# Optimization experiments

Hardware: AMD Instinct MI355X
Metric: run time of the kernel (lower is better)

Reference implementation:

```python
import jax, jax.numpy as jnp
import numpy as np

B, E, F, Q = 8, 2000, 6000, 20
D = 256   # entity_dim == word_dim (required: word_embedding output feeds LSTM with input_size=word_dim)
WD = 256
L = 3
NUM_ENTITY, NUM_REL, NUM_WORD = 400000, 6000, 60000
NNZ = 2 * B * F
PAGERANK_LAMBDA, FACT_SCALE = 0.8, 3.0
VERY_NEG = -100000000000.0
VERY_SMALL = 1e-10


def _lin(x, W, b):
    return x @ W.T + b


def _sparse_bmm(indices, values, x, num_rows):
    # indices: [3, nnz] = (batch, row, col); x: [B, C, Dx] -> out [B, num_rows, Dx]
    b, r, c = indices[0], indices[1], indices[2]
    contrib = values[:, None] * x[b, c]
    seg = b * num_rows + r
    out = jax.ops.segment_sum(contrib, seg, num_segments=x.shape[0] * num_rows)
    return out.reshape(x.shape[0], num_rows, x.shape[2])


def _lstm(x, Wih, Whh, bih, bhh):
    # PyTorch LSTM, batch_first, 1 layer, unidirectional; gate order i,f,g,o
    Bb, T, _ = x.shape
    H = Whh.shape[1]
    def step(carry, xt):
        h, c = carry
        g = xt @ Wih.T + bih + h @ Whh.T + bhh
        i, f, gg, o = jnp.split(g, 4, axis=-1)
        c = jax.nn.sigmoid(f) * c + jax.nn.sigmoid(i) * jnp.tanh(gg)
        h = jax.nn.sigmoid(o) * jnp.tanh(c)
        return (h, c), h
    init = (jnp.zeros((Bb, H), x.dtype), jnp.zeros((Bb, H), x.dtype))
    (h, c), hs = jax.lax.scan(step, init, jnp.swapaxes(x, 0, 1))
    return jnp.swapaxes(hs, 0, 1), h


def setup_inputs():
    key = jax.random.key(0)
    ks = iter(jax.random.split(key, 48))
    p = lambda shape: jax.random.normal(next(ks), shape, jnp.float32) * 0.02
    inp = {}
    inp['local_entity'] = jax.random.randint(next(ks), (B, E), 0, NUM_ENTITY + 1)
    inp['q2e_adj_mat'] = (jax.random.uniform(next(ks), (B, E, 1)) < 0.01).astype(jnp.float32)
    inp['kb_fact_rel'] = jax.random.randint(next(ks), (B, F), 0, NUM_REL)
    inp['query_text'] = jax.random.randint(next(ks), (B, Q), 0, NUM_WORD)
    inp['answer_dist'] = (jax.random.uniform(next(ks), (B, E)) < 0.005).astype(jnp.float32)
    eb = jax.random.randint(next(ks), (NNZ,), 0, B)
    ef = jax.random.randint(next(ks), (NNZ,), 0, F)
    ee = jax.random.randint(next(ks), (NNZ,), 0, E)
    inp['e2f_indices'] = jnp.stack([eb, ef, ee])
    inp['e2f_val'] = jnp.ones((NNZ,), jnp.float32)
    fb = jax.random.randint(next(ks), (NNZ,), 0, B)
    fe = jax.random.randint(next(ks), (NNZ,), 0, E)
    ff = jax.random.randint(next(ks), (NNZ,), 0, F)
    inp['f2e_indices'] = jnp.stack([fb, fe, ff])
    inp['f2e_val'] = jnp.ones((NNZ,), jnp.float32)
    inp['entity_table'] = p((NUM_ENTITY + 1, WD)).at[-1].set(0.0)
    inp['ent_lin_W'] = p((D, WD)); inp['ent_lin_b'] = jnp.zeros((D,), jnp.float32)
    inp['relation_table'] = p((NUM_REL + 1, WD)).at[-1].set(0.0)
    inp['rel_lin_W'] = p((D, WD)); inp['rel_lin_b'] = jnp.zeros((D,), jnp.float32)
    inp['word_table'] = p((NUM_WORD + 1, D)).at[-1].set(0.0)
    inp['lstm_Wih'] = p((4 * D, WD)); inp['lstm_Whh'] = p((4 * D, D))
    inp['lstm_bih'] = jnp.zeros((4 * D,), jnp.float32); inp['lstm_bhh'] = jnp.zeros((4 * D,), jnp.float32)
    inp['q2e_W'] = p((L, D, D)); inp['q2e_b'] = jnp.zeros((L, D), jnp.float32)
    inp['e2q_W'] = p((L, D, 3 * D)); inp['e2q_b'] = jnp.zeros((L, D), jnp.float32)
    inp['e2e_W'] = p((L, D, 3 * D)); inp['e2e_b'] = jnp.zeros((L, D), jnp.float32)
    inp['head_W'] = p((L, D, D)); inp['head_b'] = jnp.zeros((L, D), jnp.float32)
    inp['tail_W'] = p((L, D, D)); inp['tail_b'] = jnp.zeros((L, D), jnp.float32)
    inp['self_W'] = p((L, D, D)); inp['self_b'] = jnp.zeros((L, D), jnp.float32)
    inp['score_W'] = p((1, D)); inp['score_b'] = jnp.zeros((1,), jnp.float32)
    return inp


def reference(local_entity, q2e_adj_mat, kb_fact_rel, query_text, answer_dist, e2f_indices, e2f_val, f2e_indices, f2e_val, entity_table, ent_lin_W, ent_lin_b, relation_table, rel_lin_W, rel_lin_b, word_table, lstm_Wih, lstm_Whh, lstm_bih, lstm_bhh, q2e_W, q2e_b, e2q_W, e2q_b, e2e_W, e2e_b, head_W, head_b, tail_W, tail_b, self_W, self_b, score_W, score_b):
    query_mask = (query_text != NUM_WORD).astype(jnp.float32)          # [B,Q]
    local_entity_mask = (local_entity != NUM_ENTITY).astype(jnp.float32)
    # query encoder (dropout = identity in eval)
    query_hidden, h_last = _lstm(word_table[query_text], lstm_Wih, lstm_Whh, lstm_bih, lstm_bhh)
    query_node_emb = h_last[:, None, :]                                # [B,1,D]
    local_fact_emb = _lin(relation_table[kb_fact_rel], rel_lin_W, rel_lin_b)  # [B,F,D]
    div = jnp.sqrt(jnp.float32(D))
    sim = jnp.einsum('bqd,bfd->bqf', query_hidden, local_fact_emb) / div
    sim = jax.nn.softmax(sim + (1.0 - query_mask)[:, :, None] * VERY_NEG, axis=1)
    att = jnp.einsum('bqf,bqd->bfd', sim, query_hidden)
    Wt = jnp.sum(att * local_fact_emb, axis=2) / div                   # [B,F]
    W_tilde = jnp.exp(Wt - jnp.max(Wt, axis=1, keepdims=True))
    e2fT = jnp.stack([e2f_indices[0], e2f_indices[2], e2f_indices[1]])  # transpose(1,2)
    e2f_softmax = _sparse_bmm(e2fT, e2f_val, W_tilde[:, :, None], E)[..., 0]
    e2f_softmax = jnp.maximum(e2f_softmax, VERY_SMALL)
    pagerank_f = q2e_adj_mat[..., 0]                                    # [B,E]
    local_entity_emb = _lin(entity_table[local_entity], ent_lin_W, ent_lin_b)  # [B,E,D]
    for i in range(L):
        q2e_emb = jnp.broadcast_to(_lin(query_node_emb, q2e_W[i], q2e_b[i]), (B, E, D))
        nxt = jnp.concatenate([local_entity_emb, q2e_emb], axis=2)
        e2f_emb = jax.nn.relu(_lin(local_fact_emb, self_W[i], self_b[i]) + _sparse_bmm(e2f_indices, e2f_val, _lin(local_entity_emb, head_W[i], head_b[i]), F))
        e2f_norm = W_tilde[:, :, None] * _sparse_bmm(e2f_indices, e2f_val, (pagerank_f / e2f_softmax)[:, :, None], F)
        e2f_emb = e2f_emb * e2f_norm
        f2e_emb = jax.nn.relu(_lin(local_entity_emb, self_W[i], self_b[i]) + _sparse_bmm(f2e_indices, f2e_val, _lin(e2f_emb, tail_W[i], tail_b[i]), E))
        pagerank_f = PAGERANK_LAMBDA * _sparse_bmm(f2e_indices, f2e_val, e2f_norm, E)[..., 0] + (1.0 - PAGERANK_LAMBDA) * pagerank_f
        nxt = jnp.concatenate([nxt, FACT_SCALE * f2e_emb], axis=2)      # [B,E,3D]
        query_node_emb = jnp.einsum('be,bed->bd', pagerank_f, _lin(nxt, e2q_W[i], e2q_b[i]))[:, None, :]
        local_entity_emb = jax.nn.relu(_lin(nxt, e2e_W[i], e2e_b[i]))
    score = _lin(local_entity_emb, score_W, score_b)[..., 0]            # [B,E]
    loss = jnp.mean(jnp.maximum(score, 0.0) - score * answer_dist + jnp.log1p(jnp.exp(-jnp.abs(score))))
    score_m = score + (1.0 - local_entity_mask) * VERY_NEG
    pred = jnp.argmax(score_m, axis=1)
    pred_dist = jax.nn.sigmoid(score_m) * local_entity_mask
    return (loss, pred, pred_dist)
```

## Files before the change

kernel.cpp:

```cpp
#include <hip/hip_runtime.h>
#include <math.h>

#define BB 8
#define EE 2000
#define FF 6000
#define QQ 20
#define DD 256
#define NENT 400000
#define NWORD 60000
#define NNZ_ 96000
#define VNEG  (-1e11f)
#define VSMALL 1e-10f

typedef __attribute__((ext_vector_type(8))) short short8v;
typedef __attribute__((ext_vector_type(4))) short short4v;
typedef __attribute__((ext_vector_type(4))) float f32x4;

__device__ __forceinline__ unsigned short f2bf_rne(float x)
{
    unsigned u = __float_as_uint(x);
    u += 0x7FFFu + ((u >> 16) & 1u);
    return (unsigned short)(u >> 16);
}
__device__ __forceinline__ float bf2f(unsigned short h)
{
    return __uint_as_float((unsigned)h << 16);
}

template<int GATHER, int DUALW, int RELU, int RS, int BIASB>
__device__ __forceinline__ void mgemm_body(
    const float* __restrict__ A1, const int* __restrict__ idx,
    const float* __restrict__ A2, float sA2,
    const short* __restrict__ W1h, const short* __restrict__ W1l,
    const short* __restrict__ W2h, const short* __restrict__ W2l,
    const float* __restrict__ biasA,
    const float* __restrict__ rowscale, const float* __restrict__ bias2,
    float* __restrict__ out, int by, int bx,
    short* __restrict__ Ah, short* __restrict__ Al)
{
    const int tid = threadIdx.x;
    const int lane = tid & 63, wv = tid >> 6;
    const int wrow = wv >> 1, wcol = wv & 1;
    const int row0 = by * 128, col0 = bx * 64;

    const int sr = tid >> 1;
    const int sko = (tid & 1) << 5;
    const int grow = row0 + sr;
    const float* aRow1 = GATHER ? A1 + (size_t)idx[grow] * 256 : A1 + (size_t)grow * 256;
    const float* aRow2 = DUALW ? A2 + (size_t)grow * 256 : nullptr;

    f32x4 acc[4][2];
    #pragma unroll
    for (int i = 0; i < 4; ++i)
        #pragma unroll
        for (int j = 0; j < 2; ++j) acc[i][j] = (f32x4){0.f, 0.f, 0.f, 0.f};

    const int nch = DUALW ? 8 : 4;
    for (int ch = 0; ch < nch; ++ch) {
        const bool hi2 = DUALW && (ch >= 4);
        const float* ar = hi2 ? aRow2 : aRow1;
        const int kbase = (ch & 3) << 6;
        #pragma unroll
        for (int q = 0; q < 8; ++q) {
            const int kc = sko + (q << 2);
            float4 a = *(const float4*)(ar + kbase + kc);
            if (DUALW && hi2) { a.x *= sA2; a.y *= sA2; a.z *= sA2; a.w *= sA2; }
            unsigned short h0 = f2bf_rne(a.x), h1 = f2bf_rne(a.y),
                           h2 = f2bf_rne(a.z), h3 = f2bf_rne(a.w);
            unsigned short l0 = f2bf_rne(a.x - bf2f(h0)), l1 = f2bf_rne(a.y - bf2f(h1)),
                           l2 = f2bf_rne(a.z - bf2f(h2)), l3 = f2bf_rne(a.w - bf2f(h3));
            const int tI = ((sr >> 4) << 1) + (kc >> 5);
            const int off = (tI << 9) + ((((sr & 15)) + (((kc >> 3) & 3) << 4)) << 3) + (kc & 7);
            *(short4v*)(Ah + off) = (short4v){(short)h0, (short)h1, (short)h2, (short)h3};
            *(short4v*)(Al + off) = (short4v){(short)l0, (short)l1, (short)l2, (short)l3};
        }
        __syncthreads();
        const short* Wh = hi2 ? W2h : W1h;
        const short* Wl = hi2 ? W2l : W1l;
        #pragma unroll
        for (int ks = 0; ks < 2; ++ks) {
            const int kg = kbase + (ks << 5) + ((lane >> 4) << 3);
            short8v bh[2], bl[2];
            #pragma unroll
            for (int ct = 0; ct < 2; ++ct) {
                const int c = col0 + (wcol << 5) + (ct << 4) + (lane & 15);
                bh[ct] = *(const short8v*)(Wh + (size_t)c * 256 + kg);
                bl[ct] = *(const short8v*)(Wl + (size_t)c * 256 + kg);
            }
            #pragma unroll
            for (int rt = 0; rt < 4; ++rt) {
                const int tI = (((wrow << 2) + rt) << 1) + ks;
                const short8v avh = *(const short8v*)(Ah + (tI << 9) + (lane << 3));
                const short8v avl = *(const short8v*)(Al + (tI << 9) + (lane << 3));
                #pragma unroll
                for (int ct = 0; ct < 2; ++ct) {
                    acc[rt][ct] = __builtin_amdgcn_mfma_f32_16x16x32_bf16(avh, bh[ct], acc[rt][ct], 0, 0, 0);
                    acc[rt][ct] = __builtin_amdgcn_mfma_f32_16x16x32_bf16(avh, bl[ct], acc[rt][ct], 0, 0, 0);
                    acc[rt][ct] = __builtin_amdgcn_mfma_f32_16x16x32_bf16(avl, bh[ct], acc[rt][ct], 0, 0, 0);
                }
            }
        }
        __syncthreads();
    }
    #pragma unroll
    for (int rt = 0; rt < 4; ++rt) {
        const int rb = row0 + (wrow << 6) + (rt << 4) + ((lane >> 4) << 2);
        #pragma unroll
        for (int ct = 0; ct < 2; ++ct) {
            const int c = col0 + (wcol << 5) + (ct << 4) + (lane & 15);
            #pragma unroll
            for (int j = 0; j < 4; ++j) {
                const int r = rb + j;
                float v = acc[rt][ct][j];
                v += BIASB ? biasA[(size_t)(r / EE) * 256 + c] : biasA[c];
                if (RS) v += rowscale[r] * bias2[c];
                if (RELU) v = fmaxf(v, 0.f);
                out[(size_t)r * 256 + c] = v;
            }
        }
    }
}

template<int GATHER, int DUALW, int RELU, int RS, int BIASB>
__global__ __launch_bounds__(256, 2) void mgemm_k(
    const float* __restrict__ A1, const int* __restrict__ idx,
    const float* __restrict__ A2, float sA2,
    const short* __restrict__ W1h, const short* __restrict__ W1l,
    const short* __restrict__ W2h, const short* __restrict__ W2l,
    const float* __restrict__ biasA,
    const float* __restrict__ rowscale, const float* __restrict__ bias2,
    float* __restrict__ out)
{
    __shared__ short Ah[16 * 512];
    __shared__ short Al[16 * 512];
    mgemm_body<GATHER, DUALW, RELU, RS, BIASB>(A1, idx, A2, sA2, W1h, W1l, W2h, W2l,
        biasA, rowscale, bias2, out, blockIdx.y, blockIdx.x, Ah, Al);
}

__global__ __launch_bounds__(256, 2) void mgemm_pair_k(
    const float* __restrict__ Aa, const short* __restrict__ Wah, const short* __restrict__ Wal,
    const float* __restrict__ ba, float* __restrict__ outa, int nya,
    const float* __restrict__ Ab, const short* __restrict__ Wbh, const short* __restrict__ Wbl,
    const float* __restrict__ bb, float* __restrict__ outb)
{
    __shared__ short Ah[16 * 512];
    __shared__ short Al[16 * 512];
    const int by = blockIdx.y;
    if (by < nya)
        mgemm_body<0, 0, 0, 0, 0>(Aa, nullptr, nullptr, 1.f, Wah, Wal, nullptr, nullptr,
            ba, nullptr, nullptr, outa, by, blockIdx.x, Ah, Al);
    else
        mgemm_body<0, 0, 0, 0, 0>(Ab, nullptr, nullptr, 1.f, Wbh, Wbl, nullptr, nullptr,
            bb, nullptr, nullptr, outb, by - nya, blockIdx.x, Ah, Al);
}

__global__ void wpack_k(const float* __restrict__ relW, const float* __restrict__ entW,
                        const float* __restrict__ headW, const float* __restrict__ tailW,
                        const float* __restrict__ selfW, const float* __restrict__ e2eW,
                        short* __restrict__ wh, short* __restrict__ wl)
{
    int id = blockIdx.x * 256 + threadIdx.x;
    if (id >= 17 * 65536) return;
    int m = id >> 16, e = id & 65535;
    float x;
    if (m == 0)       x = relW[e];
    else if (m == 1)  x = entW[e];
    else if (m < 5)   x = headW[(size_t)(m - 2) * 65536 + e];
    else if (m < 8)   x = tailW[(size_t)(m - 5) * 65536 + e];
    else if (m < 11)  x = selfW[(size_t)(m - 8) * 65536 + e];
    else if (m < 14)  x = e2eW[(size_t)(m - 11) * 196608 + (size_t)(e >> 8) * 768 + (e & 255)];
    else              x = e2eW[(size_t)(m - 14) * 196608 + (size_t)(e >> 8) * 768 + 512 + (e & 255)];
    unsigned short h = f2bf_rne(x);
    wh[id] = (short)h;
    wl[id] = (short)f2bf_rne(x - bf2f(h));
}

template<int GATHER>
__global__ __launch_bounds__(256, 4) void gemm3_k(
    const float* __restrict__ A1, const int* __restrict__ idx,
    const float* __restrict__ W1, int ldw1,
    const float* __restrict__ biasA,
    float* __restrict__ out, int M, int N)
{
    __shared__ float As[16][68];
    __shared__ float Bs[16][132];
    const int tid = threadIdx.x;
    const int row0 = blockIdx.y * 64, col0 = blockIdx.x * 128;
    const int tx = tid & 15, ty = tid >> 4;
    const int srA = tid >> 2, skA = (tid & 3) << 2;
    const int srB = tid >> 1, skB = (tid & 1) << 3;
    const int grA = row0 + srA;
    const bool rvalid = (grA < M);
    const float* aRow1 = nullptr;
    if (rvalid) aRow1 = GATHER ? A1 + (size_t)idx[grA] * 256 : A1 + (size_t)grA * 256;
    const float* wR1 = W1 + (size_t)(col0 + srB) * ldw1;

    float acc[4][8];
    #pragma unroll
    for (int i = 0; i < 4; ++i)
        #pragma unroll
        for (int j = 0; j < 8; ++j) acc[i][j] = 0.f;

    float4 a0, b0, b1;
    auto fetch = [&](int ch) {
        const int k0 = ch << 4;
        if (rvalid) a0 = *(const float4*)(aRow1 + k0 + skA);
        else        a0 = make_float4(0.f, 0.f, 0.f, 0.f);
        b0 = *(const float4*)(wR1 + k0 + skB);
        b1 = *(const float4*)(wR1 + k0 + skB + 4);
    };

    fetch(0);
    for (int ch = 0; ch < 16; ++ch) {
        As[skA + 0][srA] = a0.x; As[skA + 1][srA] = a0.y;
        As[skA + 2][srA] = a0.z; As[skA + 3][srA] = a0.w;
        Bs[skB + 0][srB] = b0.x; Bs[skB + 1][srB] = b0.y;
        Bs[skB + 2][srB] = b0.z; Bs[skB + 3][srB] = b0.w;
        Bs[skB + 4][srB] = b1.x; Bs[skB + 5][srB] = b1.y;
        Bs[skB + 6][srB] = b1.z; Bs[skB + 7][srB] = b1.w;
        __syncthreads();
        if (ch + 1 < 16) fetch(ch + 1);
        #pragma unroll
        for (int kk = 0; kk < 16; ++kk) {
            float av[4], bv[8];
            *(float4*)&av[0] = *(const float4*)&As[kk][ty << 2];
            *(float4*)&bv[0] = *(const float4*)&Bs[kk][tx << 2];
            *(float4*)&bv[4] = *(const float4*)&Bs[kk][(tx << 2) + 64];
            #pragma unroll
            for (int i = 0; i < 4; ++i)
                #pragma unroll
                for (int j = 0; j < 8; ++j) acc[i][j] += av[i] * bv[j];
        }
        __syncthreads();
    }
    #pragma unroll
    for (int i = 0; i < 4; ++i) {
        int r = row0 + (ty << 2) + i;
        if (r >= M) continue;
        float* orow = out + (size_t)r * N;
        #pragma unroll
        for (int jh = 0; jh < 2; ++jh) {
            const int c = col0 + (jh << 6) + (tx << 2);
            float4 v;
            v.x = acc[i][jh * 4 + 0] + biasA[c + 0];
            v.y = acc[i][jh * 4 + 1] + biasA[c + 1];
            v.z = acc[i][jh * 4 + 2] + biasA[c + 2];
            v.w = acc[i][jh * 4 + 3] + biasA[c + 3];
            *(float4*)(orow + c) = v;
        }
    }
}

__global__ void csr_count_k(const int* __restrict__ idx, int* __restrict__ cnt, int nrPerB)
{
    int k = blockIdx.x * 256 + threadIdx.x;
    if (k >= NNZ_) return;
    atomicAdd(&cnt[idx[k] * nrPerB + idx[NNZ_ + k]], 1);
}

__global__ __launch_bounds__(1024) void scan2_k(
    const int* __restrict__ cntA, int* __restrict__ rpA, int* __restrict__ curA, int nA,
    const int* __restrict__ cntB, int* __restrict__ rpB, int* __restrict__ curB, int nB)
{
    const int* cnt = blockIdx.x ? cntB : cntA;
    int* rp  = blockIdx.x ? rpB  : rpA;
    int* cur = blockIdx.x ? curB : curA;
    int n    = blockIdx.x ? nB   : nA;
    __shared__ int sums[1024];
    int t = threadIdx.x;
    int chunk = (n + 1023) / 1024;
    int lo = t * chunk, hi = lo + chunk;
    if (lo > n) lo = n;
    if (hi > n) hi = n;
    int s = 0;
    for (int i = lo; i < hi; ++i) s += cnt[i];
    sums[t] = s;
    __syncthreads();
    for (int off = 1; off < 1024; off <<= 1) {
        int v = (t >= off) ? sums[t - off] : 0;
        __syncthreads();
        sums[t] += v;
        __syncthreads();
    }
    int run = (t == 0) ? 0 : sums[t - 1];
    for (int i = lo; i < hi; ++i) { rp[i] = run; cur[i] = run; run += cnt[i]; }
    if (hi == n) rp[n] = run;
}

__global__ void csr_fill_k(const int* __restrict__ idx, const float* __restrict__ val,
                           int* __restrict__ cur, int* __restrict__ col,
                           float* __restrict__ valp, int nrPerB)
{
    int k = blockIdx.x * 256 + threadIdx.x;
    if (k >= NNZ_) return;
    int row = idx[k] * nrPerB + idx[NNZ_ + k];
    int p = atomicAdd(&cur[row], 1);
    col[p] = idx[2 * NNZ_ + k];
    valp[p] = val[k];
}

__global__ void degw_k(const int* __restrict__ rp, const float* __restrict__ vp,
                       float* __restrict__ degw, int n)
{
    int r = blockIdx.x * 256 + threadIdx.x;
    if (r >= n) return;
    float s = 0.f;
    for (int j = rp[r]; j < rp[r + 1]; ++j) s += vp[j];
    degw[r] = s;
}

__global__ __launch_bounds__(256) void gather_fused_e2f_k(
    const int* __restrict__ rowptr, const int* __restrict__ col,
    const float* __restrict__ valp, const float* __restrict__ headsrc,
    const float* __restrict__ pr, const float* __restrict__ sm,
    const float* __restrict__ Wtil, float* __restrict__ e2fnrm,
    float* __restrict__ dst, int nrows)
{
    int gid = blockIdx.x * 256 + threadIdx.x;
    int row = gid >> 6, lane = gid & 63;
    if (row >= nrows) return;
    int b = row / FF;
    const float* prb = pr + (size_t)b * EE;
    const float* smb = sm + (size_t)b * EE;
    float4* dp = (float4*)(dst + (size_t)row * DD + (lane << 2));
    float4 acc = *dp;
    float ns = 0.f;
    int j0 = rowptr[row], j1 = rowptr[row + 1];
    for (int j = j0; j < j1; ++j) {
        int c = col[j];
        float v = valp[j];
        float4 x = *(const float4*)(headsrc + ((size_t)b * EE + c) * DD + (lane << 2));
        acc.x += v * x.x; acc.y += v * x.y; acc.z += v * x.z; acc.w += v * x.w;
        ns += v * (prb[c] / fmaxf(smb[c], VSMALL));
    }
    float nrm = Wtil[row] * ns;
    if (lane == 0) e2fnrm[row] = nrm;
    acc.x = fmaxf(acc.x, 0.f) * nrm; acc.y = fmaxf(acc.y, 0.f) * nrm;
    acc.z = fmaxf(acc.z, 0.f) * nrm; acc.w = fmaxf(acc.w, 0.f) * nrm;
    *dp = acc;
}

__global__ __launch_bounds__(256) void gather_sum_k(
    const int* __restrict__ rowptr, const int* __restrict__ col,
    const float* __restrict__ valp, const float* __restrict__ src,
    float* __restrict__ dst, int nrows, int nrPerB, int ncs)
{
    int gid = blockIdx.x * 256 + threadIdx.x;
    int row = gid >> 6, lane = gid & 63;
    if (row >= nrows) return;
    int b = row / nrPerB;
    float4 acc = make_float4(0.f, 0.f, 0.f, 0.f);
    int j0 = rowptr[row], j1 = rowptr[row + 1];
    for (int j = j0; j < j1; ++j) {
        int c = col[j];
        float v = valp[j];
        float4 x = *(const float4*)(src + ((size_t)b * ncs + c) * DD + (lane << 2));
        acc.x += v * x.x; acc.y += v * x.y; acc.z += v * x.z; acc.w += v * x.w;
    }
    *(float4*)(dst + (size_t)row * DD + (lane << 2)) = acc;
}

__global__ void transpose_whh_k(const float* __restrict__ Whh, float* __restrict__ WhhT)
{
    int i = blockIdx.x * 256 + threadIdx.x;
    int k = i >> 10, j = i & 1023;
    WhhT[i] = Whh[(size_t)j * 256 + k];
}

__global__ __launch_bounds__(256) void lstm_k(
    const float* __restrict__ Xg, const float* __restrict__ WhhT,
    const float* __restrict__ bhh, float* __restrict__ qh, float* __restrict__ qne)
{
    __shared__ float h[DD];
    __shared__ float gs[4 * DD];
    const int b = blockIdx.x, t = threadIdx.x;
    h[t] = 0.f;
    float c = 0.f;
    const float4 bb4 = *(const float4*)(bhh + 4 * t);
    const float4* wt4 = (const float4*)WhhT + t;
    __syncthreads();
    for (int step = 0; step < QQ; ++step) {
        float a0 = 0.f, a1 = 0.f, a2 = 0.f, a3 = 0.f;
        #pragma unroll 16
        for (int k = 0; k < DD; ++k) {
            float4 w = wt4[k * 256];
            float hk = h[k];
            a0 += w.x * hk; a1 += w.y * hk; a2 += w.z * hk; a3 += w.w * hk;
        }
        float4 xg = *(const float4*)(Xg + ((size_t)b * QQ + step) * 1024 + 4 * t);
        float4 g4 = make_float4(a0 + xg.x + bb4.x, a1 + xg.y + bb4.y,
                                a2 + xg.z + bb4.z, a3 + xg.w + bb4.w);
        *(float4*)(gs + 4 * t) = g4;
        __syncthreads();
        float gi = gs[t], gf = gs[DD + t], gg = gs[2 * DD + t], go = gs[3 * DD + t];
        float si = 1.f / (1.f + expf(-gi));
        float sf = 1.f / (1.f + expf(-gf));
        float so = 1.f / (1.f + expf(-go));
        c = sf * c + si * tanhf(gg);
        float hh = so * tanhf(c);
        h[t] = hh;
        qh[((size_t)b * QQ + step) * DD + t] = hh;
        __syncthreads();
    }
    qne[(size_t)b * DD + t] = h[t];
}

__global__ __launch_bounds__(256) void simwt_k(
    const float* __restrict__ qhid, const int* __restrict__ qtext,
    const float* __restrict__ lfe, float* __restrict__ Wt)
{
    __shared__ float qs[QQ * DD];
    __shared__ float qmn[QQ];
    const int b = blockIdx.y;
    const int f = blockIdx.x * 256 + threadIdx.x;
    for (int i = threadIdx.x; i < QQ * DD; i += 256) qs[i] = qhid[(size_t)b * QQ * DD + i];
    if (threadIdx.x < QQ)
        qmn[threadIdx.x] = (qtext[b * QQ + threadIdx.x] != NWORD) ? 0.f : VNEG;
    __syncthreads();
    if (f >= FF) return;
    float acc[QQ];
    #pragma unroll
    for (int q = 0; q < QQ; ++q) acc[q] = 0.f;
    const float* lr = lfe + ((size_t)b * FF + f) * DD;
    for (int d = 0; d < DD; d += 4) {
        float4 x = *(const float4*)(lr + d);
        #pragma unroll
        for (int q = 0; q < QQ; ++q) {
            float4 y = *(const float4*)&qs[q * DD + d];
            acc[q] += x.x * y.x + x.y * y.y + x.z * y.z + x.w * y.w;
        }
    }
    const float inv = 0.0625f;
    float pre[QQ], m = -INFINITY;
    #pragma unroll
    for (int q = 0; q < QQ; ++q) { pre[q] = acc[q] * inv + qmn[q]; m = fmaxf(m, pre[q]); }
    float s = 0.f;
    #pragma unroll
    for (int q = 0; q < QQ; ++q) s += expf(pre[q] - m);
    float wt = 0.f;
    #pragma unroll
    for (int q = 0; q < QQ; ++q) wt += (expf(pre[q] - m) / s) * (acc[q] * inv);
    Wt[(size_t)b * FF + f] = wt;
}

__global__ void rowmax_k(const float* __restrict__ Wt, float* __restrict__ WtMax)
{
    __shared__ float red[256];
    int b = blockIdx.x;
    float m = -INFINITY;
    for (int f = threadIdx.x; f < FF; f += 256) m = fmaxf(m, Wt[b * FF + f]);
    red[threadIdx.x] = m; __syncthreads();
    for (int s = 128; s > 0; s >>= 1) {
        if (threadIdx.x < s) red[threadIdx.x] = fmaxf(red[threadIdx.x], red[threadIdx.x + s]);
        __syncthreads();
    }
    if (threadIdx.x == 0) WtMax[b] = red[0];
}

__global__ void wtil_k(const float* __restrict__ Wt, const float* __restrict__ WtMax,
                       float* __restrict__ Wtil)
{
    int i = blockIdx.x * 256 + threadIdx.x;
    if (i >= BB * FF) return;
    Wtil[i] = expf(Wt[i] - WtMax[i / FF]);
}

__global__ void scatter_sm_k(const int* __restrict__ idx, const float* __restrict__ val,
                             const float* __restrict__ Wtil, float* __restrict__ dst)
{
    int k = blockIdx.x * 256 + threadIdx.x;
    if (k >= NNZ_) return;
    int b = idx[k], e = idx[2 * NNZ_ + k], f = idx[NNZ_ + k];
    atomicAdd(&dst[(size_t)b * EE + e], val[k] * Wtil[(size_t)b * FF + f]);
}

__global__ __launch_bounds__(256) void qlin_ebias_k(
    const float* __restrict__ qne, const float* __restrict__ q2eW,
    const float* __restrict__ q2eb, const float* __restrict__ e2eW,
    const float* __restrict__ e2eb, float* __restrict__ qlin, float* __restrict__ ebias)
{
    __shared__ float xs[DD], qs[DD];
    int b = blockIdx.x, j = threadIdx.x;
    xs[j] = qne[b * DD + j];
    __syncthreads();
    float acc = q2eb[j];
    const float* wr = q2eW + (size_t)j * DD;
    #pragma unroll 4
    for (int k = 0; k < DD; ++k) acc += xs[k] * wr[k];
    qlin[b * DD + j] = acc;
    qs[j] = acc;
    __syncthreads();
    float acc2 = e2eb[j];
    const float* wr2 = e2eW + (size_t)j * 768 + 256;
    #pragma unroll 4
    for (int k = 0; k < DD; ++k) acc2 += qs[k] * wr2[k];
    ebias[b * DD + j] = acc2;
}

#define VCH 80
#define NCHK (EE / VCH)
__global__ __launch_bounds__(256) void vreduce_pr_k(
    const int* __restrict__ f2e_rp, const int* __restrict__ f2e_col,
    const float* __restrict__ f2e_vp, const float* __restrict__ e2fnrm,
    float* __restrict__ pr, const float* __restrict__ lee,
    const float* __restrict__ f2e, float* __restrict__ vpartL,
    float* __restrict__ vpartF, float* __restrict__ vpartS)
{
    int b = blockIdx.y, ch = blockIdx.x, k = threadIdx.x;
    int e0 = ch * VCH;
    __shared__ float prs[VCH];
    if (k < VCH) {
        int row = b * EE + e0 + k;
        float s = 0.f;
        for (int j = f2e_rp[row]; j < f2e_rp[row + 1]; ++j)
            s += f2e_vp[j] * e2fnrm[(size_t)b * FF + f2e_col[j]];
        float v = 0.8f * s + 0.2f * pr[row];
        pr[row] = v;
        prs[k] = v;
    }
    __syncthreads();
    float a1 = 0.f, a2 = 0.f;
    for (int e = 0; e < VCH; ++e) {
        float p = prs[e];
        size_t base = ((size_t)b * EE + e0 + e) * DD + k;
        a1 += p * lee[base];
        a2 += p * f2e[base];
    }
    int pi = ch * BB + b;
    vpartL[(size_t)pi * DD + k] = a1;
    vpartF[(size_t)pi * DD + k] = a2;
    float sp = 0.f;
    for (int e = k; e < VCH; e += 256) sp += prs[e];
    __shared__ float red[256];
    red[k] = sp; __syncthreads();
    for (int s = 128; s > 0; s >>= 1) {
        if (k < s) red[k] += red[k + s];
        __syncthreads();
    }
    if (k == 0) vpartS[pi] = red[0];
}

__global__ __launch_bounds__(256) void qneupd_qlin_k(
    const float* __restrict__ vpartL, const float* __restrict__ vpartF,
    const float* __restrict__ vpartS, const float* __restrict__ qlinCur,
    const float* __restrict__ W, const float* __restrict__ bias,
    float* __restrict__ qne,
    const float* __restrict__ q2eWn, const float* __restrict__ q2ebn,
    const float* __restrict__ e2eWn, const float* __restrict__ e2ebn,
    float* __restrict__ qlinNext, float* __restrict__ ebiasNext, int hasNext)
{
    __shared__ float s1[DD], s2[DD], s3[DD], qn[DD], qs[DD];
    int b = blockIdx.x, j = threadIdx.x;
    float a1 = 0.f, a3 = 0.f, sp = 0.f;
    for (int ch = 0; ch < NCHK; ++ch) {
        int pi = ch * BB + b;
        a1 += vpartL[(size_t)pi * DD + j];
        a3 += vpartF[(size_t)pi * DD + j];
        sp += vpartS[pi];
    }
    s1[j] = a1; s2[j] = qlinCur[b * DD + j]; s3[j] = a3;
    __syncthreads();
    float acc = sp * bias[j];
    const float* wr = W + (size_t)j * 768;
    #pragma unroll 4
    for (int k = 0; k < DD; ++k)
        acc += s1[k] * wr[k] + sp * s2[k] * wr[256 + k] + 3.f * s3[k] * wr[512 + k];
    qne[b * DD + j] = acc;
    if (!hasNext) return;
    qn[j] = acc;
    __syncthreads();
    float aq = q2ebn[j];
    const float* wq = q2eWn + (size_t)j * DD;
    #pragma unroll 4
    for (int k = 0; k < DD; ++k) aq += qn[k] * wq[k];
    qlinNext[b * DD + j] = aq;
    qs[j] = aq;
    __syncthreads();
    float ae = e2ebn[j];
    const float* we = e2eWn + (size_t)j * 768 + 256;
    #pragma unroll 4
    for (int k = 0; k < DD; ++k) ae += qs[k] * we[k];
    ebiasNext[b * DD + j] = ae;
}

__global__ void score_k(const float* __restrict__ lee, const float* __restrict__ sw,
                        const float* __restrict__ sb, float* __restrict__ score)
{
    int r = blockIdx.x * 256 + threadIdx.x;
    if (r >= BB * EE) return;
    float acc = sb[0];
    const float* a = lee + (size_t)r * DD;
    for (int k = 0; k < DD; k += 4) {
        float4 v = *(const float4*)(a + k);
        acc += v.x * sw[k] + v.y * sw[k + 1] + v.z * sw[k + 2] + v.w * sw[k + 3];
    }
    score[r] = acc;
}

__global__ __launch_bounds__(256) void final_k(
    const float* __restrict__ score, const int* __restrict__ local_entity,
    const float* __restrict__ ans, float* __restrict__ out, float* __restrict__ losspart)
{
    int b = blockIdx.x, t = threadIdx.x;
    float lsum = 0.f, bm = -INFINITY;
    int bi = EE;
    for (int e = t; e < EE; e += 256) {
        float s = score[b * EE + e];
        float mask = (local_entity[b * EE + e] != NENT) ? 1.f : 0.f;
        float smv = s + (1.f - mask) * VNEG;
        float sig;
        if (smv >= 0.f) sig = 1.f / (1.f + expf(-smv));
        else { float es = expf(smv); sig = es / (1.f + es); }
        out[1 + BB + b * EE + e] = sig * mask;
        lsum += fmaxf(s, 0.f) - s * ans[b * EE + e] + log1pf(expf(-fabsf(s)));
        if (smv > bm) { bm = smv; bi = e; }
    }
    __shared__ float rv[256]; __shared__ int ri[256]; __shared__ float rl[256];
    rv[t] = bm; ri[t] = bi; rl[t] = lsum;
    __syncthreads();
    for (int s = 128; s > 0; s >>= 1) {
        if (t < s) {
            rl[t] += rl[t + s];
            if (rv[t + s] > rv[t] || (rv[t + s] == rv[t] && ri[t + s] < ri[t])) {
                rv[t] = rv[t + s]; ri[t] = ri[t + s];
            }
        }
        __syncthreads();
    }
    if (t == 0) { losspart[b] = rl[0]; out[1 + b] = (float)ri[0]; }
}

__global__ void loss_k(const float* __restrict__ losspart, float* __restrict__ out)
{
    if (threadIdx.x == 0) {
        float s = 0.f;
        for (int b = 0; b < BB; ++b) s += losspart[b];
        out[0] = s / (float)(BB * EE);
    }
}

extern "C" void kernel_launch(void* const* d_in, const int* in_sizes, int n_in,
                              void* d_out, int out_size, void* d_ws, size_t ws_size,
                              hipStream_t stream)
{
    (void)in_sizes; (void)n_in; (void)out_size; (void)ws_size;
    const int*   local_entity = (const int*)d_in[0];
    const float* q2e_adj      = (const float*)d_in[1];
    const int*   kb_fact_rel  = (const int*)d_in[2];
    const int*   query_text   = (const int*)d_in[3];
    const float* answer_dist  = (const float*)d_in[4];
    const int*   e2f_idx      = (const int*)d_in[5];
    const float* e2f_val      = (const float*)d_in[6];
    const int*   f2e_idx      = (const int*)d_in[7];
    const float* f2e_val      = (const float*)d_in[8];
    const float* entity_table = (const float*)d_in[9];
    const float* ent_W        = (const float*)d_in[10];
    const float* ent_b        = (const float*)d_in[11];
    const float* rel_table    = (const float*)d_in[12];
    const float* rel_W        = (const float*)d_in[13];
    const float* rel_b        = (const float*)d_in[14];
    const float* word_table   = (const float*)d_in[15];
    const float* Wih          = (const float*)d_in[16];
    const float* Whh          = (const float*)d_in[17];
    const float* bih          = (const float*)d_in[18];
    const float* bhh          = (const float*)d_in[19];
    const float* q2e_W        = (const float*)d_in[20];
    const float* q2e_b        = (const float*)d_in[21];
    const float* e2q_W        = (const float*)d_in[22];
    const float* e2q_b        = (const float*)d_in[23];
    const float* e2e_W        = (const float*)d_in[24];
    const float* e2e_b        = (const float*)d_in[25];
    const float* head_W       = (const float*)d_in[26];
    const float* head_b       = (const float*)d_in[27];
    const float* tail_W       = (const float*)d_in[28];
    const float* tail_b       = (const float*)d_in[29];
    const float* self_W       = (const float*)d_in[30];
    const float* self_b       = (const float*)d_in[31];
    const float* score_W      = (const float*)d_in[32];
    const float* score_b      = (const float*)d_in[33];

    const int NR1 = BB * FF;
    const int NR2 = BB * EE;

    float* ws = (float*)d_ws;
    size_t off = 0;
    auto alloc = [&](size_t n) { float* p = ws + off; off += n; return p; };
    float* Xg      = alloc((size_t)BB * QQ * 1024);
    float* WhhT    = alloc((size_t)1024 * DD);
    float* qh      = alloc((size_t)BB * QQ * DD);
    float* qne     = alloc(BB * DD);
    float* lfe     = alloc((size_t)NR1 * DD);
    float* lee     = alloc((size_t)NR2 * DD);
    float* lee2    = alloc((size_t)NR2 * DD);
    float* Wt      = alloc(BB * FF);
    float* WtMax   = alloc(8);
    float* Wtil    = alloc(BB * FF);
    float* e2fsm   = alloc(BB * EE);
    float* pr      = alloc(BB * EE);
    float* qlinA   = alloc(BB * DD);
    float* qlinB   = alloc(BB * DD);
    float* ebiasA  = alloc(BB * DD);
    float* ebiasB  = alloc(BB * DD);
    float* e2fnrm  = alloc(BB * FF);
    float* scoreb  = alloc(BB * EE);
    float* losspart= alloc(8);
    float* bufC    = alloc((size_t)NR2 * DD);
    float* e2fT    = alloc((size_t)NR1 * DD);
    float* f2eT    = alloc((size_t)NR2 * DD);
    float* tmp     = alloc((size_t)NR2 * DD);
    float* vpartL  = alloc((size_t)NCHK * BB * DD);
    float* vpartF  = alloc((size_t)NCHK * BB * DD);
    float* vpartS  = alloc(NCHK * BB);
    float* degw2   = alloc(NR2);
    float* e2f_vp  = alloc(NNZ_);
    float* f2e_vp  = alloc(NNZ_);
    short* wbh = (short*)alloc(17 * 65536 / 2);
    short* wbl = (short*)alloc(17 * 65536 / 2);
    int* ib = (int*)(ws + off);
    size_t ioff = 0;
    auto ialloc = [&](size_t n) { int* p = ib + ioff; ioff += n; return p; };
    int* e2f_cnt = ialloc(NR1);
    int* e2f_rp  = ialloc(NR1 + 1);
    int* e2f_cur = ialloc(NR1);
    int* e2f_col = ialloc(NNZ_);
    int* f2e_cnt = ialloc(NR2);
    int* f2e_rp  = ialloc(NR2 + 1);
    int* f2e_cur = ialloc(NR2);
    int* f2e_col = ialloc(NNZ_);

    auto WH = [&](int m) { return wbh + (size_t)m * 65536; };
    auto WL = [&](int m) { return wbl + (size_t)m * 65536; };

    float* outp = (float*)d_out;
    const int SCB = (NNZ_ + 255) / 256;

    wpack_k<<<(17 * 65536) / 256, 256, 0, stream>>>(rel_W, ent_W, head_W, tail_W,
                                                    self_W, e2e_W, wbh, wbl);

    hipMemsetAsync(e2f_cnt, 0, NR1 * sizeof(int), stream);
    hipMemsetAsync(f2e_cnt, 0, NR2 * sizeof(int), stream);
    csr_count_k<<<SCB, 256, 0, stream>>>(e2f_idx, e2f_cnt, FF);
    csr_count_k<<<SCB, 256, 0, stream>>>(f2e_idx, f2e_cnt, EE);
    scan2_k<<<2, 1024, 0, stream>>>(e2f_cnt, e2f_rp, e2f_cur, NR1,
                                    f2e_cnt, f2e_rp, f2e_cur, NR2);
    csr_fill_k<<<SCB, 256, 0, stream>>>(e2f_idx, e2f_val, e2f_cur, e2f_col, e2f_vp, FF);
    csr_fill_k<<<SCB, 256, 0, stream>>>(f2e_idx, f2e_val, f2e_cur, f2e_col, f2e_vp, EE);
    degw_k<<<(NR2 + 255) / 256, 256, 0, stream>>>(f2e_rp, f2e_vp, degw2, NR2);

    gemm3_k<1><<<dim3(8, 3), 256, 0, stream>>>(
        word_table, query_text, Wih, 256, bih, Xg, BB * QQ, 1024);
    transpose_whh_k<<<1024, 256, 0, stream>>>(Whh, WhhT);
    lstm_k<<<BB, 256, 0, stream>>>(Xg, WhhT, bhh, qh, qne);

    mgemm_k<1, 0, 0, 0, 0><<<dim3(4, 375), 256, 0, stream>>>(
        rel_table, kb_fact_rel, nullptr, 1.f, WH(0), WL(0), nullptr, nullptr,
        rel_b, nullptr, nullptr, lfe);
    mgemm_k<1, 0, 0, 0, 0><<<dim3(4, 125), 256, 0, stream>>>(
        entity_table, local_entity, nullptr, 1.f, WH(1), WL(1), nullptr, nullptr,
        ent_b, nullptr, nullptr, lee);

    simwt_k<<<dim3((FF + 255) / 256, BB), 256, 0, stream>>>(qh, query_text, lfe, Wt);
    rowmax_k<<<BB, 256, 0, stream>>>(Wt, WtMax);
    wtil_k<<<(BB * FF + 255) / 256, 256, 0, stream>>>(Wt, WtMax, Wtil);

    hipMemsetAsync(e2fsm, 0, BB * EE * sizeof(float), stream);
    scatter_sm_k<<<SCB, 256, 0, stream>>>(e2f_idx, e2f_val, Wtil, e2fsm);

    hipMemcpyAsync(pr, q2e_adj, BB * EE * sizeof(float), hipMemcpyDeviceToDevice, stream);
    qlin_ebias_k<<<BB, 256, 0, stream>>>(qne, q2e_W, q2e_b, e2e_W, e2e_b, qlinA, ebiasA);

    float* qlinCur = qlinA;  float* qlinNxt = qlinB;
    float* ebiasCur = ebiasA; float* ebiasNxt = ebiasB;

    for (int i = 0; i < 3; ++i) {
        const float* e2qWi  = e2q_W  + (size_t)i * DD * 3 * DD;
        const float* e2qbi  = e2q_b  + i * DD;
        const float* headbi = head_b + i * DD;
        const float* tailbi = tail_b + i * DD;
        const float* selfbi = self_b + i * DD;

        mgemm_pair_k<<<dim3(4, 125 + 375), 256, 0, stream>>>(
            lee, WH(2 + i), WL(2 + i), headbi, bufC, 125,
            lfe, WH(8 + i), WL(8 + i), selfbi, e2fT);

        gather_fused_e2f_k<<<(NR1 * 64) / 256, 256, 0, stream>>>(
            e2f_rp, e2f_col, e2f_vp, bufC, pr, e2fsm, Wtil, e2fnrm, e2fT, NR1);

        gather_sum_k<<<(NR2 * 64) / 256, 256, 0, stream>>>(
            f2e_rp, f2e_col, f2e_vp, e2fT, tmp, NR2, EE, FF);

        mgemm_k<0, 1, 1, 1, 0><<<dim3(4, 125), 256, 0, stream>>>(
            lee, nullptr, tmp, 1.f, WH(8 + i), WL(8 + i), WH(5 + i), WL(5 + i),
            selfbi, degw2, tailbi, f2eT);

        vreduce_pr_k<<<dim3(NCHK, BB), 256, 0, stream>>>(
            f2e_rp, f2e_col, f2e_vp, e2fnrm, pr, lee, f2eT, vpartL, vpartF, vpartS);

        int hasNext = (i < 2) ? 1 : 0;
        const float* q2eWn = q2e_W + (size_t)(i + 1) * DD * DD * (hasNext ? 1 : 0);
        const float* q2ebn = q2e_b + (i + 1) * DD * (hasNext ? 1 : 0);
        const float* e2eWn = e2e_W + (size_t)(i + 1) * DD * 3 * DD * (hasNext ? 1 : 0);
        const float* e2ebn = e2e_b + (i + 1) * DD * (hasNext ? 1 : 0);
        qneupd_qlin_k<<<BB, 256, 0, stream>>>(
            vpartL, vpartF, vpartS, qlinCur, e2qWi, e2qbi, qne,
            q2eWn, q2ebn, e2eWn, e2ebn, qlinNxt, ebiasNxt, hasNext);

        mgemm_k<0, 1, 1, 0, 1><<<dim3(4, 125), 256, 0, stream>>>(
            lee, nullptr, f2eT, 3.f, WH(11 + i), WL(11 + i), WH(14 + i), WL(14 + i),
            ebiasCur, nullptr, nullptr, lee2);
        { float* t = lee; lee = lee2; lee2 = t; }
        { float* t = qlinCur; qlinCur = qlinNxt; qlinNxt = t; }
        { float* t = ebiasCur; ebiasCur = ebiasNxt; ebiasNxt = t; }
    }

    score_k<<<(BB * EE + 255) / 256, 256, 0, stream>>>(lee, score_W, score_b, scoreb);
    final_k<<<BB, 256, 0, stream>>>(scoreb, local_entity, answer_dist, outp, losspart);
    loss_k<<<1, 64, 0, stream>>>(losspart, outp);
}
```

Measured before the change: 1.295 ms.

## Merge small kernels, pair embedding GEMMs, and raise GEMM occupancy bound

Several small launches are merged: the CSR count and fill passes for both adjacencies, rowmax with the softmax exponent, the two embedding-lookup GEMMs via a templated gather pair kernel, and score with the final reduction. The GEMM launch bounds go from two to four blocks per SM to push occupancy. The goal is less launch overhead and more concurrency. The risks are register spills under the tighter launch bound, and a final kernel with only 8 blocks now doing the full score dot products serially.

```diff
diff --git a/kernel.cpp b/kernel.cpp
--- a/kernel.cpp
+++ b/kernel.cpp
@@ -122,7 +122,7 @@
 }
 
 template<int GATHER, int DUALW, int RELU, int RS, int BIASB>
-__global__ __launch_bounds__(256, 2) void mgemm_k(
+__global__ __launch_bounds__(256, 4) void mgemm_k(
     const float* __restrict__ A1, const int* __restrict__ idx,
     const float* __restrict__ A2, float sA2,
     const short* __restrict__ W1h, const short* __restrict__ W1l,
@@ -137,20 +137,23 @@
         biasA, rowscale, bias2, out, blockIdx.y, blockIdx.x, Ah, Al);
 }
 
-__global__ __launch_bounds__(256, 2) void mgemm_pair_k(
-    const float* __restrict__ Aa, const short* __restrict__ Wah, const short* __restrict__ Wal,
+template<int GATHER>
+__global__ __launch_bounds__(256, 4) void mgemm_pair_k(
+    const float* __restrict__ Aa, const int* __restrict__ idxA,
+    const short* __restrict__ Wah, const short* __restrict__ Wal,
     const float* __restrict__ ba, float* __restrict__ outa, int nya,
-    const float* __restrict__ Ab, const short* __restrict__ Wbh, const short* __restrict__ Wbl,
+    const float* __restrict__ Ab, const int* __restrict__ idxB,
+    const short* __restrict__ Wbh, const short* __restrict__ Wbl,
     const float* __restrict__ bb, float* __restrict__ outb)
 {
     __shared__ short Ah[16 * 512];
     __shared__ short Al[16 * 512];
     const int by = blockIdx.y;
     if (by < nya)
-        mgemm_body<0, 0, 0, 0, 0>(Aa, nullptr, nullptr, 1.f, Wah, Wal, nullptr, nullptr,
+        mgemm_body<GATHER, 0, 0, 0, 0>(Aa, idxA, nullptr, 1.f, Wah, Wal, nullptr, nullptr,
             ba, nullptr, nullptr, outa, by, blockIdx.x, Ah, Al);
     else
-        mgemm_body<0, 0, 0, 0, 0>(Ab, nullptr, nullptr, 1.f, Wbh, Wbl, nullptr, nullptr,
+        mgemm_body<GATHER, 0, 0, 0, 0>(Ab, idxB, nullptr, 1.f, Wbh, Wbl, nullptr, nullptr,
             bb, nullptr, nullptr, outb, by - nya, blockIdx.x, Ah, Al);
 }
 
@@ -251,11 +254,13 @@
     }
 }
 
-__global__ void csr_count_k(const int* __restrict__ idx, int* __restrict__ cnt, int nrPerB)
+__global__ void csr_count2_k(const int* __restrict__ idxA, int* __restrict__ cntA,
+                             const int* __restrict__ idxB, int* __restrict__ cntB)
 {
     int k = blockIdx.x * 256 + threadIdx.x;
     if (k >= NNZ_) return;
-    atomicAdd(&cnt[idx[k] * nrPerB + idx[NNZ_ + k]], 1);
+    if (blockIdx.y == 0) atomicAdd(&cntA[idxA[k] * FF + idxA[NNZ_ + k]], 1);
+    else                 atomicAdd(&cntB[idxB[k] * EE + idxB[NNZ_ + k]], 1);
 }
 
 __global__ __launch_bounds__(1024) void scan2_k(
@@ -287,16 +292,25 @@
     if (hi == n) rp[n] = run;
 }
 
-__global__ void csr_fill_k(const int* __restrict__ idx, const float* __restrict__ val,
-                           int* __restrict__ cur, int* __restrict__ col,
-                           float* __restrict__ valp, int nrPerB)
+__global__ void csr_fill2_k(
+    const int* __restrict__ idxA, const float* __restrict__ valA,
+    int* __restrict__ curA, int* __restrict__ colA, float* __restrict__ vpA,
+    const int* __restrict__ idxB, const float* __restrict__ valB,
+    int* __restrict__ curB, int* __restrict__ colB, float* __restrict__ vpB)
 {
     int k = blockIdx.x * 256 + threadIdx.x;
     if (k >= NNZ_) return;
-    int row = idx[k] * nrPerB + idx[NNZ_ + k];
-    int p = atomicAdd(&cur[row], 1);
-    col[p] = idx[2 * NNZ_ + k];
-    valp[p] = val[k];
+    if (blockIdx.y == 0) {
+        int row = idxA[k] * FF + idxA[NNZ_ + k];
+        int p = atomicAdd(&curA[row], 1);
+        colA[p] = idxA[2 * NNZ_ + k];
+        vpA[p] = valA[k];
+    } else {
+        int row = idxB[k] * EE + idxB[NNZ_ + k];
+        int p = atomicAdd(&curB[row], 1);
+        colB[p] = idxB[2 * NNZ_ + k];
+        vpB[p] = valB[k];
+    }
 }
 
 __global__ void degw_k(const int* __restrict__ rp, const float* __restrict__ vp,
@@ -443,26 +457,20 @@
     Wt[(size_t)b * FF + f] = wt;
 }
 
-__global__ void rowmax_k(const float* __restrict__ Wt, float* __restrict__ WtMax)
+__global__ __launch_bounds__(256) void rowmax_wtil_k(
+    const float* __restrict__ Wt, float* __restrict__ Wtil)
 {
     __shared__ float red[256];
-    int b = blockIdx.x;
+    int b = blockIdx.x, t = threadIdx.x;
     float m = -INFINITY;
-    for (int f = threadIdx.x; f < FF; f += 256) m = fmaxf(m, Wt[b * FF + f]);
-    red[threadIdx.x] = m; __syncthreads();
+    for (int f = t; f < FF; f += 256) m = fmaxf(m, Wt[b * FF + f]);
+    red[t] = m; __syncthreads();
     for (int s = 128; s > 0; s >>= 1) {
-        if (threadIdx.x < s) red[threadIdx.x] = fmaxf(red[threadIdx.x], red[threadIdx.x + s]);
-        __syncthreads();
-    }
-    if (threadIdx.x == 0) WtMax[b] = red[0];
-}
-
-__global__ void wtil_k(const float* __restrict__ Wt, const float* __restrict__ WtMax,
-                       float* __restrict__ Wtil)
-{
-    int i = blockIdx.x * 256 + threadIdx.x;
-    if (i >= BB * FF) return;
-    Wtil[i] = expf(Wt[i] - WtMax[i / FF]);
+        if (t < s) red[t] = fmaxf(red[t], red[t + s]);
+        __syncthreads();
+    }
+    float mx = red[0];
+    for (int f = t; f < FF; f += 256) Wtil[b * FF + f] = expf(Wt[b * FF + f] - mx);
 }
 
 __global__ void scatter_sm_k(const int* __restrict__ idx, const float* __restrict__ val,
@@ -583,29 +591,25 @@
     ebiasNext[b * DD + j] = ae;
 }
 
-__global__ void score_k(const float* __restrict__ lee, const float* __restrict__ sw,
-                        const float* __restrict__ sb, float* __restrict__ score)
-{
-    int r = blockIdx.x * 256 + threadIdx.x;
-    if (r >= BB * EE) return;
-    float acc = sb[0];
-    const float* a = lee + (size_t)r * DD;
-    for (int k = 0; k < DD; k += 4) {
-        float4 v = *(const float4*)(a + k);
-        acc += v.x * sw[k] + v.y * sw[k + 1] + v.z * sw[k + 2] + v.w * sw[k + 3];
-    }
-    score[r] = acc;
-}
-
-__global__ __launch_bounds__(256) void final_k(
-    const float* __restrict__ score, const int* __restrict__ local_entity,
+__global__ __launch_bounds__(256) void final2_k(
+    const float* __restrict__ lee, const float* __restrict__ sw_,
+    const float* __restrict__ sb, const int* __restrict__ local_entity,
     const float* __restrict__ ans, float* __restrict__ out, float* __restrict__ losspart)
 {
+    __shared__ float sw[DD];
     int b = blockIdx.x, t = threadIdx.x;
+    sw[t] = sw_[t];
+    __syncthreads();
+    float sb0 = sb[0];
     float lsum = 0.f, bm = -INFINITY;
     int bi = EE;
     for (int e = t; e < EE; e += 256) {
-        float s = score[b * EE + e];
+        const float* a = lee + ((size_t)b * EE + e) * DD;
+        float s = sb0;
+        for (int k = 0; k < DD; k += 4) {
+            float4 v = *(const float4*)(a + k);
+            s += v.x * sw[k] + v.y * sw[k + 1] + v.z * sw[k + 2] + v.w * sw[k + 3];
+        }
         float mask = (local_entity[b * EE + e] != NENT) ? 1.f : 0.f;
         float smv = s + (1.f - mask) * VNEG;
         float sig;
@@ -685,15 +689,15 @@
     float* ws = (float*)d_ws;
     size_t off = 0;
     auto alloc = [&](size_t n) { float* p = ws + off; off += n; return p; };
+    auto salloc = [&](size_t nshorts) { short* p = (short*)(ws + off); off += nshorts / 2; return p; };
     float* Xg      = alloc((size_t)BB * QQ * 1024);
     float* WhhT    = alloc((size_t)1024 * DD);
     float* qh      = alloc((size_t)BB * QQ * DD);
     float* qne     = alloc(BB * DD);
     float* lfe     = alloc((size_t)NR1 * DD);
-    float* lee     = alloc((size_t)NR2 * DD);
-    float* lee2    = alloc((size_t)NR2 * DD);
+    float* leeA    = alloc((size_t)NR2 * DD);
+    float* leeB    = alloc((size_t)NR2 * DD);
     float* Wt      = alloc(BB * FF);
-    float* WtMax   = alloc(8);
     float* Wtil    = alloc(BB * FF);
     float* e2fsm   = alloc(BB * EE);
     float* pr      = alloc(BB * EE);
@@ -702,7 +706,6 @@
     float* ebiasA  = alloc(BB * DD);
     float* ebiasB  = alloc(BB * DD);
     float* e2fnrm  = alloc(BB * FF);
-    float* scoreb  = alloc(BB * EE);
     float* losspart= alloc(8);
     float* bufC    = alloc((size_t)NR2 * DD);
     float* e2fT    = alloc((size_t)NR1 * DD);
@@ -714,8 +717,8 @@
     float* degw2   = alloc(NR2);
     float* e2f_vp  = alloc(NNZ_);
     float* f2e_vp  = alloc(NNZ_);
-    short* wbh = (short*)alloc(17 * 65536 / 2);
-    short* wbl = (short*)alloc(17 * 65536 / 2);
+    short* wbh     = salloc((size_t)17 * 65536);
+    short* wbl     = salloc((size_t)17 * 65536);
     int* ib = (int*)(ws + off);
     size_t ioff = 0;
     auto ialloc = [&](size_t n) { int* p = ib + ioff; ioff += n; return p; };
@@ -739,12 +742,12 @@
 
     hipMemsetAsync(e2f_cnt, 0, NR1 * sizeof(int), stream);
     hipMemsetAsync(f2e_cnt, 0, NR2 * sizeof(int), stream);
-    csr_count_k<<<SCB, 256, 0, stream>>>(e2f_idx, e2f_cnt, FF);
-    csr_count_k<<<SCB, 256, 0, stream>>>(f2e_idx, f2e_cnt, EE);
+    csr_count2_k<<<dim3(SCB, 2), 256, 0, stream>>>(e2f_idx, e2f_cnt, f2e_idx, f2e_cnt);
     scan2_k<<<2, 1024, 0, stream>>>(e2f_cnt, e2f_rp, e2f_cur, NR1,
                                     f2e_cnt, f2e_rp, f2e_cur, NR2);
-    csr_fill_k<<<SCB, 256, 0, stream>>>(e2f_idx, e2f_val, e2f_cur, e2f_col, e2f_vp, FF);
-    csr_fill_k<<<SCB, 256, 0, stream>>>(f2e_idx, f2e_val, f2e_cur, f2e_col, f2e_vp, EE);
+    csr_fill2_k<<<dim3(SCB, 2), 256, 0, stream>>>(
+        e2f_idx, e2f_val, e2f_cur, e2f_col, e2f_vp,
+        f2e_idx, f2e_val, f2e_cur, f2e_col, f2e_vp);
     degw_k<<<(NR2 + 255) / 256, 256, 0, stream>>>(f2e_rp, f2e_vp, degw2, NR2);
 
     gemm3_k<1><<<dim3(8, 3), 256, 0, stream>>>(
@@ -752,16 +755,12 @@
     transpose_whh_k<<<1024, 256, 0, stream>>>(Whh, WhhT);
     lstm_k<<<BB, 256, 0, stream>>>(Xg, WhhT, bhh, qh, qne);
 
-    mgemm_k<1, 0, 0, 0, 0><<<dim3(4, 375), 256, 0, stream>>>(
-        rel_table, kb_fact_rel, nullptr, 1.f, WH(0), WL(0), nullptr, nullptr,
-        rel_b, nullptr, nullptr, lfe);
-    mgemm_k<1, 0, 0, 0, 0><<<dim3(4, 125), 256, 0, stream>>>(
-        entity_table, local_entity, nullptr, 1.f, WH(1), WL(1), nullptr, nullptr,
-        ent_b, nullptr, nullptr, lee);
+    mgemm_pair_k<1><<<dim3(4, 375 + 125), 256, 0, stream>>>(
+        rel_table, kb_fact_rel, WH(0), WL(0), rel_b, lfe, 375,
+        entity_table, local_entity, WH(1), WL(1), ent_b, leeA);
 
     simwt_k<<<dim3((FF + 255) / 256, BB), 256, 0, stream>>>(qh, query_text, lfe, Wt);
-    rowmax_k<<<BB, 256, 0, stream>>>(Wt, WtMax);
-    wtil_k<<<(BB * FF + 255) / 256, 256, 0, stream>>>(Wt, WtMax, Wtil);
+    rowmax_wtil_k<<<BB, 256, 0, stream>>>(Wt, Wtil);
 
     hipMemsetAsync(e2fsm, 0, BB * EE * sizeof(float), stream);
     scatter_sm_k<<<SCB, 256, 0, stream>>>(e2f_idx, e2f_val, Wtil, e2fsm);
@@ -769,6 +768,7 @@
     hipMemcpyAsync(pr, q2e_adj, BB * EE * sizeof(float), hipMemcpyDeviceToDevice, stream);
     qlin_ebias_k<<<BB, 256, 0, stream>>>(qne, q2e_W, q2e_b, e2e_W, e2e_b, qlinA, ebiasA);
 
+    float* lee = leeA;   float* lee2 = leeB;
     float* qlinCur = qlinA;  float* qlinNxt = qlinB;
     float* ebiasCur = ebiasA; float* ebiasNxt = ebiasB;
 
@@ -779,9 +779,9 @@
         const float* tailbi = tail_b + i * DD;
         const float* selfbi = self_b + i * DD;
 
-        mgemm_pair_k<<<dim3(4, 125 + 375), 256, 0, stream>>>(
-            lee, WH(2 + i), WL(2 + i), headbi, bufC, 125,
-            lfe, WH(8 + i), WL(8 + i), selfbi, e2fT);
+        mgemm_pair_k<0><<<dim3(4, 125 + 375), 256, 0, stream>>>(
+            lee, nullptr, WH(2 + i), WL(2 + i), headbi, bufC, 125,
+            lfe, nullptr, WH(8 + i), WL(8 + i), selfbi, e2fT);
 
         gather_fused_e2f_k<<<(NR1 * 64) / 256, 256, 0, stream>>>(
             e2f_rp, e2f_col, e2f_vp, bufC, pr, e2fsm, Wtil, e2fnrm, e2fT, NR1);
@@ -813,7 +813,7 @@
         { float* t = ebiasCur; ebiasCur = ebiasNxt; ebiasNxt = t; }
     }
 
-    score_k<<<(BB * EE + 255) / 256, 256, 0, stream>>>(lee, score_W, score_b, scoreb);
-    final_k<<<BB, 256, 0, stream>>>(scoreb, local_entity, answer_dist, outp, losspart);
+    final2_k<<<BB, 256, 0, stream>>>(lee, score_W, score_b, local_entity,
+                                     answer_dist, outp, losspart);
     loss_k<<<1, 64, 0, stream>>>(losspart, outp);
 }
```

Result: slower. 1.347 ms (+4.0%).
